# Kernel tuning notes

Measured on AMD Instinct MI355X. Metric: run time of the kernel, lower is better.

The kernel has to match this reference:

```python
import jax, jax.numpy as jnp
import numpy as np

N_NODES = 100000
N_EDGES = 1600000


def _deg_norm(idx, n):
    deg = jax.ops.segment_sum(jnp.ones(idx.shape[0], jnp.float32), idx, num_segments=n)
    return jnp.where(deg > 0, jax.lax.rsqrt(jnp.maximum(deg, 1.0)), 0.0)


def gcn_layer(src, dst, x, W, b):
    # DGL GraphConv, norm='both': D_in^{-1/2} A D_out^{-1/2} X W + b
    n = x.shape[0]
    h = x @ W                                   # project first (in >= out)
    norm_src = _deg_norm(src, n)                # out-degree norm at source
    norm_dst = _deg_norm(dst, n)                # in-degree norm at destination
    msg = (h * norm_src[:, None])[src]          # [E, d] gather
    agg = jax.ops.segment_sum(msg, dst, num_segments=n)
    return agg * norm_dst[:, None] + b


def setup_inputs() -> dict:
    key = jax.random.key(0)
    ks = jax.random.split(key, 6)
    in_f, h_f, n_cls = 256, 128, 64
    feat = jax.random.normal(ks[0], (N_NODES, in_f), jnp.float32)
    src = jax.random.randint(ks[1], (N_EDGES,), 0, N_NODES, jnp.int32)
    dst = jax.random.randint(ks[2], (N_EDGES,), 0, N_NODES, jnp.int32)
    W1 = jax.random.normal(ks[3], (in_f, h_f), jnp.float32) / np.sqrt(in_f)
    b1 = jnp.zeros((h_f,), jnp.float32)
    W2 = jax.random.normal(ks[4], (h_f, n_cls), jnp.float32) / np.sqrt(h_f)
    b2 = jnp.zeros((n_cls,), jnp.float32)
    return {"feat": feat, "src": src, "dst": dst, "W1": W1, "b1": b1, "W2": W2, "b2": b2}


def reference(feat, src, dst, W1, b1, W2, b2):
    h = gcn_layer(src, dst, feat, W1, b1)
    h = jax.nn.relu(h)
    h = gcn_layer(src, dst, h, W2, b2)
    return jax.nn.sigmoid(h)
```

## Files before the change

### kernel.cpp

```cpp
#include <hip/hip_runtime.h>
#include <cmath>

#define IN_F 256
#define H_F  128
#define N_CLS 64
#define SCAN_CHUNK 2048
#define EPB 4096
#define MAXBK 400

typedef __attribute__((ext_vector_type(8))) short bf16x8;
typedef __attribute__((ext_vector_type(4))) float f32x4;

__device__ __forceinline__ ushort f2bf(float x) {
  unsigned b = __builtin_bit_cast(unsigned, x);
  b += 0x7FFF + ((b >> 16) & 1);
  return (ushort)(b >> 16);
}

__global__ void conv_wT(const float* __restrict__ W, ushort* __restrict__ WT, int K, int N) {
  int i = blockIdx.x * blockDim.x + threadIdx.x;
  if (i >= K * N) return;
  int k = i / N, n = i % N;
  WT[n * K + k] = f2bf(W[i]);
}

__global__ __launch_bounds__(256) void hist_kernel(const int* __restrict__ src,
                                                   const int* __restrict__ dst,
                                                   int* __restrict__ hist,
                                                   int NBK, int NBLK, int E) {
  __shared__ int hD[MAXBK], hS[MAXBK];
  int t = threadIdx.x, blk = blockIdx.x;
  for (int b = t; b < NBK; b += 256) { hD[b] = 0; hS[b] = 0; }
  __syncthreads();
  int e0 = blk * EPB;
#pragma unroll
  for (int j = 0; j < EPB / 256; ++j) {
    int idx = e0 + j * 256 + t;
    if (idx < E) {
      atomicAdd(&hD[dst[idx] >> 8], 1);
      atomicAdd(&hS[src[idx] >> 8], 1);
    }
  }
  __syncthreads();
  for (int b = t; b < NBK; b += 256) {
    hist[(size_t)b * NBLK + blk] = hD[b];
    hist[(size_t)(NBK + b) * NBLK + blk] = hS[b];
  }
}

__device__ void excl_scan_lds(int* cnt, int* pos, int t, int nbk) {
  for (int b = t; b < nbk; b += 256) pos[b] = cnt[b];
  __syncthreads();
  for (int d = 1; d < 256; d <<= 1) {
    int u = (t < nbk && t >= d) ? pos[t - d] : 0;
    __syncthreads();
    if (t < nbk && t >= d) pos[t] += u;
    __syncthreads();
  }
  int m2 = nbk - 256;
  int s0 = (m2 > 0) ? pos[255] : 0;
  for (int d = 1; d < 256; d <<= 1) {
    int u = (m2 > 0 && t < m2 && t >= d) ? pos[256 + t - d] : 0;
    __syncthreads();
    if (m2 > 0 && t < m2 && t >= d) pos[256 + t] += u;
    __syncthreads();
  }
  if (m2 > 0 && t < m2) pos[256 + t] += s0;
  __syncthreads();
  for (int b = t; b < nbk; b += 256) pos[b] -= cnt[b];
  __syncthreads();
}

__global__ __launch_bounds__(256) void scatter_kernel(const int* __restrict__ src,
                                                      const int* __restrict__ dst,
                                                      const int* __restrict__ P,
                                                      int2* __restrict__ pairs_d,
                                                      int* __restrict__ srcs_s,
                                                      int NBK, int NBLK, int E) {
  __shared__ int cnt[MAXBK], pos[MAXBK], cur[MAXBK], gb[MAXBK];
  __shared__ int2 stage[EPB];
  int t = threadIdx.x, blk = blockIdx.x;
  int e0 = blk * EPB;
  int ne = E - e0; if (ne > EPB) ne = EPB;

  for (int b = t; b < NBK; b += 256) cnt[b] = 0;
  __syncthreads();
#pragma unroll
  for (int j = 0; j < EPB / 256; ++j) {
    int idx = e0 + j * 256 + t;
    if (idx < E) atomicAdd(&cnt[dst[idx] >> 8], 1);
  }
  __syncthreads();
  excl_scan_lds(cnt, pos, t, NBK);
  for (int b = t; b < NBK; b += 256) { cur[b] = pos[b]; gb[b] = P[(size_t)b * NBLK + blk]; }
  __syncthreads();
#pragma unroll
  for (int j = 0; j < EPB / 256; ++j) {
    int idx = e0 + j * 256 + t;
    if (idx < E) {
      int d = dst[idx];
      int r = atomicAdd(&cur[d >> 8], 1);
      stage[r] = make_int2(src[idx], d);
    }
  }
  __syncthreads();
  for (int i = t; i < ne; i += 256) {
    int2 p = stage[i];
    int b = p.y >> 8;
    pairs_d[gb[b] + (i - pos[b])] = p;
  }
  __syncthreads();

  int* stage_i = (int*)stage;
  for (int b = t; b < NBK; b += 256) cnt[b] = 0;
  __syncthreads();
#pragma unroll
  for (int j = 0; j < EPB / 256; ++j) {
    int idx = e0 + j * 256 + t;
    if (idx < E) atomicAdd(&cnt[src[idx] >> 8], 1);
  }
  __syncthreads();
  excl_scan_lds(cnt, pos, t, NBK);
  for (int b = t; b < NBK; b += 256) {
    cur[b] = pos[b];
    gb[b] = P[(size_t)(NBK + b) * NBLK + blk] - E;
  }
  __syncthreads();
#pragma unroll
  for (int j = 0; j < EPB / 256; ++j) {
    int idx = e0 + j * 256 + t;
    if (idx < E) {
      int s = src[idx];
      int r = atomicAdd(&cur[s >> 8], 1);
      stage_i[r] = s;
    }
  }
  __syncthreads();
  for (int i = t; i < ne; i += 256) {
    int s = stage_i[i];
    int b = s >> 8;
    srcs_s[gb[b] + (i - pos[b])] = s;
  }
}

__global__ __launch_bounds__(256) void csr_bucket(const int2* __restrict__ pairs_d,
                                                  const int* __restrict__ P,
                                                  int* __restrict__ row_off,
                                                  float* __restrict__ norm_d,
                                                  int* __restrict__ csr,
                                                  int NBK, int NBLK, int N, int E) {
  __shared__ int cnt[256], pos[256], cur[256];
  int b = blockIdx.x, t = threadIdx.x;
  int bstart = P[(size_t)b * NBLK];
  int bend = (b + 1 < NBK) ? P[(size_t)(b + 1) * NBLK] : E;
  cnt[t] = 0;
  __syncthreads();
  for (int i = bstart + t; i < bend; i += 256) atomicAdd(&cnt[pairs_d[i].y & 255], 1);
  __syncthreads();
  pos[t] = cnt[t];
  __syncthreads();
  for (int d = 1; d < 256; d <<= 1) {
    int u = (t >= d) ? pos[t - d] : 0;
    __syncthreads();
    if (t >= d) pos[t] += u;
    __syncthreads();
  }
  int excl = pos[t] - cnt[t];
  int node = b * 256 + t;
  if (node < N) {
    row_off[node] = bstart + excl;
    norm_d[node] = cnt[t] > 0 ? rsqrtf((float)cnt[t]) : 0.f;
  }
  if (b == NBK - 1 && t == 255) row_off[N] = E;
  cur[t] = excl;
  __syncthreads();
  for (int i = bstart + t; i < bend; i += 256) {
    int2 p = pairs_d[i];
    int r = atomicAdd(&cur[p.y & 255], 1);
    csr[bstart + r] = p.x;
  }
}

__global__ __launch_bounds__(256) void outdeg_bucket(const int* __restrict__ srcs_s,
                                                     const int* __restrict__ P,
                                                     float* __restrict__ norm_s,
                                                     int NBK, int NBLK, int N, int E) {
  __shared__ int cnt[256];
  int b = blockIdx.x, t = threadIdx.x;
  size_t SOFF = (size_t)NBK * NBLK;
  int sstart = P[SOFF + (size_t)b * NBLK] - E;
  int send = (b + 1 < NBK) ? P[SOFF + (size_t)(b + 1) * NBLK] - E : E;
  cnt[t] = 0;
  __syncthreads();
  for (int i = sstart + t; i < send; i += 256) atomicAdd(&cnt[srcs_s[i] & 255], 1);
  __syncthreads();
  int node = b * 256 + t;
  if (node < N) norm_s[node] = cnt[t] > 0 ? rsqrtf((float)cnt[t]) : 0.f;
}

__global__ void scan_part(const int* __restrict__ arr, int* __restrict__ bsum, int len) {
  int base = blockIdx.x * SCAN_CHUNK + threadIdx.x * 8;
  int s = 0;
#pragma unroll
  for (int j = 0; j < 8; ++j) {
    int i = base + j;
    if (i < len) s += arr[i];
  }
#pragma unroll
  for (int d = 1; d < 64; d <<= 1) s += __shfl_xor(s, d);
  __shared__ int ws[4];
  int lane = threadIdx.x & 63, w = threadIdx.x >> 6;
  if (lane == 0) ws[w] = s;
  __syncthreads();
  if (threadIdx.x == 0) bsum[blockIdx.x] = ws[0] + ws[1] + ws[2] + ws[3];
}

__global__ __launch_bounds__(1024) void scan_bsum(int* __restrict__ bsum, int nb) {
  __shared__ int sm[1024];
  int t = threadIdx.x;
  sm[t] = (t < nb) ? bsum[t] : 0;
  __syncthreads();
  for (int d = 1; d < 1024; d <<= 1) {
    int v = (t >= d) ? sm[t - d] : 0;
    __syncthreads();
    sm[t] += v;
    __syncthreads();
  }
  if (t < nb) bsum[t] = (t == 0) ? 0 : sm[t - 1];
}

__global__ void scan_final(const int* __restrict__ arr, const int* __restrict__ bsum_ex,
                           int* __restrict__ outp, int len, int total) {
  int base = blockIdx.x * SCAN_CHUNK + threadIdx.x * 8;
  int v[8], pre[8];
  int s = 0;
#pragma unroll
  for (int j = 0; j < 8; ++j) {
    int i = base + j;
    v[j] = (i < len) ? arr[i] : 0;
    pre[j] = s;
    s += v[j];
  }
  int lane = threadIdx.x & 63, w = threadIdx.x >> 6;
  int inc = s;
#pragma unroll
  for (int d = 1; d < 64; d <<= 1) {
    int u = __shfl_up(inc, d);
    if (lane >= d) inc += u;
  }
  __shared__ int wsum[4], woff[4];
  if (lane == 63) wsum[w] = inc;
  __syncthreads();
  if (threadIdx.x == 0) {
    int r = 0;
    for (int q = 0; q < 4; ++q) { woff[q] = r; r += wsum[q]; }
  }
  __syncthreads();
  int ex = (inc - s) + woff[w] + bsum_ex[blockIdx.x];
#pragma unroll
  for (int j = 0; j < 8; ++j) {
    int i = base + j;
    if (i < len) outp[i] = ex + pre[j];
  }
  if (blockIdx.x == 0 && threadIdx.x == 0) outp[len] = total;
}

__global__ __launch_bounds__(256) void mfma_gemm1(
    const float* __restrict__ A, const ushort* __restrict__ BT,
    const float* __restrict__ scale, ushort* __restrict__ C, int M) {
  constexpr int BM = 128, BN = 128, KTOT = 256, BK = 64, WM = 2, WN = 2;
  constexpr int FM = (BM / WM) / 16;
  constexpr int FN = (BN / WN) / 16;
  constexpr int ABYTES = BM * BK * 2;
  constexpr int BBYTES = BN * BK * 2;
  __shared__ char lds[ABYTES + BBYTES];
  char* Asm = lds;
  char* Bsm = lds + ABYTES;

  const int tid = threadIdx.x;
  const int lane = tid & 63;
  const int w = tid >> 6;
  const int wm = w / WN, wn = w % WN;
  const int m0 = blockIdx.x * BM;

  f32x4 acc[FM][FN];
#pragma unroll
  for (int m = 0; m < FM; ++m)
#pragma unroll
    for (int n = 0; n < FN; ++n) acc[m][n] = (f32x4){0.f, 0.f, 0.f, 0.f};

  const int ra = lane & 15;
  const int kg = lane >> 4;

  for (int kt = 0; kt < KTOT / BK; ++kt) {
#pragma unroll
    for (int s = 0; s < ABYTES / 4096; ++s) {
      int L = s * 4096 + tid * 16;
      int r = L >> 7;
      int slot = (L >> 4) & 7;
      int gr = m0 + r; if (gr >= M) gr = M - 1;
      const float4* gp = (const float4*)(A + (size_t)gr * KTOT + kt * BK + slot * 8);
      float4 va = gp[0], vb = gp[1];
      bf16x8 o;
      o[0] = (short)f2bf(va.x); o[1] = (short)f2bf(va.y);
      o[2] = (short)f2bf(va.z); o[3] = (short)f2bf(va.w);
      o[4] = (short)f2bf(vb.x); o[5] = (short)f2bf(vb.y);
      o[6] = (short)f2bf(vb.z); o[7] = (short)f2bf(vb.w);
      *(bf16x8*)(Asm + (L ^ ((r & 7) << 4))) = o;
    }
#pragma unroll
    for (int s = 0; s < BBYTES / 4096; ++s) {
      int L = s * 4096 + tid * 16;
      int r = L >> 7;
      int slot = (L >> 4) & 7;
      const char* gp = (const char*)BT + (size_t)r * (KTOT * 2) + kt * (BK * 2)
                     + ((slot * 16) ^ ((r & 7) << 4));
      __builtin_amdgcn_global_load_lds(
          (const __attribute__((address_space(1))) unsigned*)gp,
          (__attribute__((address_space(3))) unsigned*)(Bsm + L), 16, 0, 0);
    }
    __syncthreads();

#pragma unroll
    for (int ks = 0; ks < 2; ++ks) {
      bf16x8 af[FM], bfr[FN];
#pragma unroll
      for (int m = 0; m < FM; ++m) {
        int r = wm * (BM / WM) + m * 16 + ra;
        int cb = ks * 64 + kg * 16;
        af[m] = *(const bf16x8*)(Asm + r * 128 + (cb ^ ((r & 7) << 4)));
      }
#pragma unroll
      for (int n = 0; n < FN; ++n) {
        int c = wn * (BN / WN) + n * 16 + ra;
        int cb = ks * 64 + kg * 16;
        bfr[n] = *(const bf16x8*)(Bsm + c * 128 + (cb ^ ((c & 7) << 4)));
      }
#pragma unroll
      for (int m = 0; m < FM; ++m)
#pragma unroll
        for (int n = 0; n < FN; ++n)
          acc[m][n] = __builtin_amdgcn_mfma_f32_16x16x32_bf16(af[m], bfr[n], acc[m][n], 0, 0, 0);
    }
    __syncthreads();
  }

#pragma unroll
  for (int m = 0; m < FM; ++m) {
#pragma unroll
    for (int j = 0; j < 4; ++j) {
      int rl = wm * (BM / WM) + m * 16 + (lane >> 4) * 4 + j;
      int gr = m0 + rl;
      if (gr < M) {
        float sc = scale[gr];
#pragma unroll
        for (int n = 0; n < FN; ++n) {
          int c = wn * (BN / WN) + n * 16 + (lane & 15);
          C[(size_t)gr * BN + c] = f2bf(acc[m][n][j] * sc);
        }
      }
    }
  }
}

template<int BM, int BN, int KTOT, int WM, int WN>
__global__ __launch_bounds__(256) void mfma_gemm_scale(
    const ushort* __restrict__ A, const ushort* __restrict__ BT,
    const float* __restrict__ scale, ushort* __restrict__ C, int M) {
  constexpr int BK = 64;
  constexpr int FM = (BM / WM) / 16;
  constexpr int FN = (BN / WN) / 16;
  constexpr int ABYTES = BM * BK * 2;
  constexpr int BBYTES = BN * BK * 2;
  __shared__ char lds[ABYTES + BBYTES];
  char* Asm = lds;
  char* Bsm = lds + ABYTES;

  const int tid = threadIdx.x;
  const int lane = tid & 63;
  const int w = tid >> 6;
  const int wm = w / WN, wn = w % WN;
  const int m0 = blockIdx.x * BM;

  f32x4 acc[FM][FN];
#pragma unroll
  for (int m = 0; m < FM; ++m)
#pragma unroll
    for (int n = 0; n < FN; ++n) acc[m][n] = (f32x4){0.f, 0.f, 0.f, 0.f};

  const int ra = lane & 15;
  const int kg = lane >> 4;

  for (int kt = 0; kt < KTOT / BK; ++kt) {
#pragma unroll
    for (int s = 0; s < ABYTES / 4096; ++s) {
      int L = s * 4096 + tid * 16;
      int r = L >> 7;
      int slot = (L >> 4) & 7;
      int gr = m0 + r; if (gr >= M) gr = M - 1;
      const char* gp = (const char*)A + (size_t)gr * (KTOT * 2) + kt * (BK * 2)
                     + ((slot * 16) ^ ((r & 7) << 4));
      __builtin_amdgcn_global_load_lds(
          (const __attribute__((address_space(1))) unsigned*)gp,
          (__attribute__((address_space(3))) unsigned*)(Asm + L), 16, 0, 0);
    }
#pragma unroll
    for (int s = 0; s < BBYTES / 4096; ++s) {
      int L = s * 4096 + tid * 16;
      int r = L >> 7;
      int slot = (L >> 4) & 7;
      const char* gp = (const char*)BT + (size_t)r * (KTOT * 2) + kt * (BK * 2)
                     + ((slot * 16) ^ ((r & 7) << 4));
      __builtin_amdgcn_global_load_lds(
          (const __attribute__((address_space(1))) unsigned*)gp,
          (__attribute__((address_space(3))) unsigned*)(Bsm + L), 16, 0, 0);
    }
    __syncthreads();

#pragma unroll
    for (int ks = 0; ks < 2; ++ks) {
      bf16x8 af[FM], bfr[FN];
#pragma unroll
      for (int m = 0; m < FM; ++m) {
        int r = wm * (BM / WM) + m * 16 + ra;
        int cb = ks * 64 + kg * 16;
        af[m] = *(const bf16x8*)(Asm + r * 128 + (cb ^ ((r & 7) << 4)));
      }
#pragma unroll
      for (int n = 0; n < FN; ++n) {
        int c = wn * (BN / WN) + n * 16 + ra;
        int cb = ks * 64 + kg * 16;
        bfr[n] = *(const bf16x8*)(Bsm + c * 128 + (cb ^ ((c & 7) << 4)));
      }
#pragma unroll
      for (int m = 0; m < FM; ++m)
#pragma unroll
        for (int n = 0; n < FN; ++n)
          acc[m][n] = __builtin_amdgcn_mfma_f32_16x16x32_bf16(af[m], bfr[n], acc[m][n], 0, 0, 0);
    }
    __syncthreads();
  }

#pragma unroll
  for (int m = 0; m < FM; ++m) {
#pragma unroll
    for (int j = 0; j < 4; ++j) {
      int rl = wm * (BM / WM) + m * 16 + (lane >> 4) * 4 + j;
      int gr = m0 + rl;
      if (gr < M) {
        float sc = scale[gr];
#pragma unroll
        for (int n = 0; n < FN; ++n) {
          int c = wn * (BN / WN) + n * 16 + (lane & 15);
          C[(size_t)gr * BN + c] = f2bf(acc[m][n][j] * sc);
        }
      }
    }
  }
}

__global__ void gather1(const ushort* __restrict__ h1, const int* __restrict__ off,
                        const int* __restrict__ csr, const float* __restrict__ nd,
                        const float* __restrict__ b1, ushort* __restrict__ x2, int N) {
  int w = (blockIdx.x * blockDim.x + threadIdx.x) >> 6;
  int lane = threadIdx.x & 63;
  if (w >= N) return;
  int lo = off[w], hi = off[w + 1];
  const unsigned* h = (const unsigned*)h1;
  float sx = 0.f, sy = 0.f;
#define ACC1(u) { sx += __builtin_bit_cast(float, (u) << 16); \
                  sy += __builtin_bit_cast(float, (u) & 0xFFFF0000u); }
  int j = lo;
  for (; j + 16 <= hi; j += 16) {
    int s0 = csr[j+0], s1 = csr[j+1], s2 = csr[j+2], s3 = csr[j+3];
    int s4 = csr[j+4], s5 = csr[j+5], s6 = csr[j+6], s7 = csr[j+7];
    int s8 = csr[j+8], s9 = csr[j+9], sa = csr[j+10], sb = csr[j+11];
    int sc_ = csr[j+12], sd = csr[j+13], se = csr[j+14], sf = csr[j+15];
    unsigned u0 = h[(size_t)s0 * 64 + lane];
    unsigned u1 = h[(size_t)s1 * 64 + lane];
    unsigned u2 = h[(size_t)s2 * 64 + lane];
    unsigned u3 = h[(size_t)s3 * 64 + lane];
    unsigned u4 = h[(size_t)s4 * 64 + lane];
    unsigned u5 = h[(size_t)s5 * 64 + lane];
    unsigned u6 = h[(size_t)s6 * 64 + lane];
    unsigned u7 = h[(size_t)s7 * 64 + lane];
    unsigned u8 = h[(size_t)s8 * 64 + lane];
    unsigned u9 = h[(size_t)s9 * 64 + lane];
    unsigned ua = h[(size_t)sa * 64 + lane];
    unsigned ub = h[(size_t)sb * 64 + lane];
    unsigned uc = h[(size_t)sc_ * 64 + lane];
    unsigned ud = h[(size_t)sd * 64 + lane];
    unsigned ue = h[(size_t)se * 64 + lane];
    unsigned uf = h[(size_t)sf * 64 + lane];
    ACC1(u0) ACC1(u1) ACC1(u2) ACC1(u3) ACC1(u4) ACC1(u5) ACC1(u6) ACC1(u7)
    ACC1(u8) ACC1(u9) ACC1(ua) ACC1(ub) ACC1(uc) ACC1(ud) ACC1(ue) ACC1(uf)
  }
  for (; j + 4 <= hi; j += 4) {
    int s0 = csr[j+0], s1 = csr[j+1], s2 = csr[j+2], s3 = csr[j+3];
    unsigned u0 = h[(size_t)s0 * 64 + lane];
    unsigned u1 = h[(size_t)s1 * 64 + lane];
    unsigned u2 = h[(size_t)s2 * 64 + lane];
    unsigned u3 = h[(size_t)s3 * 64 + lane];
    ACC1(u0) ACC1(u1) ACC1(u2) ACC1(u3)
  }
  for (; j < hi; ++j) {
    int s = csr[j];
    unsigned u = h[(size_t)s * 64 + lane];
    ACC1(u)
  }
#undef ACC1
  float sc = nd[w];
  float2 bb = ((const float2*)b1)[lane];
  float ox = fmaxf(sx * sc + bb.x, 0.f);
  float oy = fmaxf(sy * sc + bb.y, 0.f);
  ushort2 o; o.x = f2bf(ox); o.y = f2bf(oy);
  ((ushort2*)x2)[(size_t)w * 64 + lane] = o;
}

__global__ void gather2(const ushort* __restrict__ h2, const int* __restrict__ off,
                        const int* __restrict__ csr, const float* __restrict__ nd,
                        const float* __restrict__ b2, float* __restrict__ out, int N) {
  int wv = (blockIdx.x * blockDim.x + threadIdx.x) >> 6;
  int lane = threadIdx.x & 63;
  int grp = lane >> 5;
  int sub = lane & 31;
  int node = wv * 2 + grp;
  if (node >= N) return;
  int lo = off[node], hi = off[node + 1];
  const unsigned* h = (const unsigned*)h2;
  float s0f = 0.f, s1f = 0.f;
#define ACC2(u) { s0f += __builtin_bit_cast(float, (u) << 16); \
                  s1f += __builtin_bit_cast(float, (u) & 0xFFFF0000u); }
  int j = lo;
  for (; j + 16 <= hi; j += 16) {
    int i0 = csr[j+0], i1 = csr[j+1], i2 = csr[j+2], i3 = csr[j+3];
    int i4 = csr[j+4], i5 = csr[j+5], i6 = csr[j+6], i7 = csr[j+7];
    int i8 = csr[j+8], i9 = csr[j+9], ia = csr[j+10], ib = csr[j+11];
    int ic = csr[j+12], id = csr[j+13], ie = csr[j+14], if_ = csr[j+15];
    unsigned u0 = h[(size_t)i0 * 32 + sub];
    unsigned u1 = h[(size_t)i1 * 32 + sub];
    unsigned u2 = h[(size_t)i2 * 32 + sub];
    unsigned u3 = h[(size_t)i3 * 32 + sub];
    unsigned u4 = h[(size_t)i4 * 32 + sub];
    unsigned u5 = h[(size_t)i5 * 32 + sub];
    unsigned u6 = h[(size_t)i6 * 32 + sub];
    unsigned u7 = h[(size_t)i7 * 32 + sub];
    unsigned u8 = h[(size_t)i8 * 32 + sub];
    unsigned u9 = h[(size_t)i9 * 32 + sub];
    unsigned ua = h[(size_t)ia * 32 + sub];
    unsigned ub = h[(size_t)ib * 32 + sub];
    unsigned uc = h[(size_t)ic * 32 + sub];
    unsigned ud = h[(size_t)id * 32 + sub];
    unsigned ue = h[(size_t)ie * 32 + sub];
    unsigned uf = h[(size_t)if_ * 32 + sub];
    ACC2(u0) ACC2(u1) ACC2(u2) ACC2(u3) ACC2(u4) ACC2(u5) ACC2(u6) ACC2(u7)
    ACC2(u8) ACC2(u9) ACC2(ua) ACC2(ub) ACC2(uc) ACC2(ud) ACC2(ue) ACC2(uf)
  }
  for (; j + 4 <= hi; j += 4) {
    int i0 = csr[j+0], i1 = csr[j+1], i2 = csr[j+2], i3 = csr[j+3];
    unsigned u0 = h[(size_t)i0 * 32 + sub];
    unsigned u1 = h[(size_t)i1 * 32 + sub];
    unsigned u2 = h[(size_t)i2 * 32 + sub];
    unsigned u3 = h[(size_t)i3 * 32 + sub];
    ACC2(u0) ACC2(u1) ACC2(u2) ACC2(u3)
  }
  for (; j < hi; ++j) {
    int i0 = csr[j];
    unsigned u = h[(size_t)i0 * 32 + sub];
    ACC2(u)
  }
#undef ACC2
  float scn = nd[node];
  float2 bb = ((const float2*)b2)[sub];
  float v0 = s0f * scn + bb.x;
  float v1 = s1f * scn + bb.y;
  float2 o;
  o.x = 1.f / (1.f + expf(-v0));
  o.y = 1.f / (1.f + expf(-v1));
  ((float2*)out)[(size_t)node * 32 + sub] = o;
}

extern "C" void kernel_launch(void* const* d_in, const int* in_sizes, int n_in,
                              void* d_out, int out_size, void* d_ws, size_t ws_size,
                              hipStream_t stream) {
  const float* feat = (const float*)d_in[0];
  const int*   src  = (const int*)d_in[1];
  const int*   dst  = (const int*)d_in[2];
  const float* W1   = (const float*)d_in[3];
  const float* b1   = (const float*)d_in[4];
  const float* W2   = (const float*)d_in[5];
  const float* b2   = (const float*)d_in[6];
  float* out = (float*)d_out;

  const int N = in_sizes[0] / IN_F;
  const int E = in_sizes[1];

  const int NBK  = (N + 255) >> 8;
  const int NBLK = (E + EPB - 1) / EPB;
  const int HLEN = 2 * NBK * NBLK;

  size_t off = 0;
  auto alloc = [&](size_t bytes) -> void* {
    void* p = (char*)d_ws + off;
    off = (off + bytes + 255) & ~(size_t)255;
    return p;
  };
  int*    hist    = (int*)alloc((size_t)HLEN * 4);
  int*    P       = (int*)alloc((size_t)(HLEN + 1) * 4);
  int*    bsum    = (int*)alloc((size_t)1024 * 4);
  int2*   pairs_d = (int2*)alloc((size_t)E * 8);
  int*    srcs_s  = (int*)alloc((size_t)E * 4);
  float*  norm_s  = (float*)alloc((size_t)N * 4);
  float*  norm_d  = (float*)alloc((size_t)N * 4);
  int*    row_off = (int*)alloc((size_t)(N + 1) * 4);
  int*    csr     = (int*)alloc((size_t)E * 4);
  ushort* w1t     = (ushort*)alloc((size_t)H_F * IN_F * 2);
  ushort* w2t     = (ushort*)alloc((size_t)N_CLS * H_F * 2);
  ushort* h1      = (ushort*)alloc((size_t)N * H_F * 2);
  ushort* x2bf    = (ushort*)alloc((size_t)N * H_F * 2);
  ushort* h2      = (ushort*)alloc((size_t)N * N_CLS * 2);
  (void)ws_size;

  conv_wT<<<(IN_F * H_F + 255) / 256, 256, 0, stream>>>(W1, w1t, IN_F, H_F);
  conv_wT<<<(H_F * N_CLS + 255) / 256, 256, 0, stream>>>(W2, w2t, H_F, N_CLS);

  hist_kernel<<<NBLK, 256, 0, stream>>>(src, dst, hist, NBK, NBLK, E);
  const int NBS = (HLEN + SCAN_CHUNK - 1) / SCAN_CHUNK;
  scan_part<<<NBS, 256, 0, stream>>>(hist, bsum, HLEN);
  scan_bsum<<<1, 1024, 0, stream>>>(bsum, NBS);
  scan_final<<<NBS, 256, 0, stream>>>(hist, bsum, P, HLEN, 2 * E);
  scatter_kernel<<<NBLK, 256, 0, stream>>>(src, dst, P, pairs_d, srcs_s, NBK, NBLK, E);
  csr_bucket<<<NBK, 256, 0, stream>>>(pairs_d, P, row_off, norm_d, csr, NBK, NBLK, N, E);
  outdeg_bucket<<<NBK, 256, 0, stream>>>(srcs_s, P, norm_s, NBK, NBLK, N, E);

  mfma_gemm1<<<(N + 127) / 128, 256, 0, stream>>>(feat, w1t, norm_s, h1, N);
  gather1<<<(N * 64 + 255) / 256, 256, 0, stream>>>(h1, row_off, csr, norm_d, b1, x2bf, N);

  mfma_gemm_scale<128, 64, 128, 2, 2><<<(N + 127) / 128, 256, 0, stream>>>(
      x2bf, w2t, norm_s, h2, N);
  int pairs = (N + 1) / 2;
  gather2<<<(pairs * 64 + 255) / 256, 256, 0, stream>>>(h2, row_off, csr, norm_d, b2, out, N);
}
```

Before: 229.1 us.

## Pack edge pairs, merge bucket kernels, and split layer-1 gather into feature halves

The sorted edge pairs are packed into one 32-bit word (source index shifted left by 8, low byte of destination), which halves scatter and CSR-build traffic. The in-degree and out-degree bucket kernels become one launch, as do the two weight conversions. The layer-1 gather now runs in two passes, each covering half the feature columns with two nodes per wavefront. This shrinks the per-pass working set of h1 to improve cache hit rate, at the cost of reading the CSR twice. The packing assumes source indices fit in 24 bits.

```diff
diff --git a/kernel.cpp b/kernel.cpp
--- a/kernel.cpp
+++ b/kernel.cpp
@@ -17,11 +17,17 @@
   return (ushort)(b >> 16);
 }
 
-__global__ void conv_wT(const float* __restrict__ W, ushort* __restrict__ WT, int K, int N) {
+__global__ void conv_w(const float* __restrict__ W1, ushort* __restrict__ W1T,
+                       const float* __restrict__ W2, ushort* __restrict__ W2T) {
   int i = blockIdx.x * blockDim.x + threadIdx.x;
-  if (i >= K * N) return;
-  int k = i / N, n = i % N;
-  WT[n * K + k] = f2bf(W[i]);
+  if (i < IN_F * H_F) {
+    int k = i / H_F, n = i % H_F;
+    W1T[n * IN_F + k] = f2bf(W1[i]);
+  } else if (i < IN_F * H_F + H_F * N_CLS) {
+    int j = i - IN_F * H_F;
+    int k = j / N_CLS, n = j % N_CLS;
+    W2T[n * H_F + k] = f2bf(W2[j]);
+  }
 }
 
 __global__ __launch_bounds__(256) void hist_kernel(const int* __restrict__ src,
@@ -74,11 +80,12 @@
 __global__ __launch_bounds__(256) void scatter_kernel(const int* __restrict__ src,
                                                       const int* __restrict__ dst,
                                                       const int* __restrict__ P,
-                                                      int2* __restrict__ pairs_d,
+                                                      int* __restrict__ pairs_pk,
                                                       int* __restrict__ srcs_s,
                                                       int NBK, int NBLK, int E) {
   __shared__ int cnt[MAXBK], pos[MAXBK], cur[MAXBK], gb[MAXBK];
-  __shared__ int2 stage[EPB];
+  __shared__ int stage_pk[EPB];
+  __shared__ ushort stage_b[EPB];
   int t = threadIdx.x, blk = blockIdx.x;
   int e0 = blk * EPB;
   int ne = E - e0; if (ne > EPB) ne = EPB;
@@ -100,18 +107,17 @@
     if (idx < E) {
       int d = dst[idx];
       int r = atomicAdd(&cur[d >> 8], 1);
-      stage[r] = make_int2(src[idx], d);
+      stage_pk[r] = (src[idx] << 8) | (d & 255);
+      stage_b[r] = (ushort)(d >> 8);
     }
   }
   __syncthreads();
   for (int i = t; i < ne; i += 256) {
-    int2 p = stage[i];
-    int b = p.y >> 8;
-    pairs_d[gb[b] + (i - pos[b])] = p;
-  }
-  __syncthreads();
-
-  int* stage_i = (int*)stage;
+    int b = stage_b[i];
+    pairs_pk[gb[b] + (i - pos[b])] = stage_pk[i];
+  }
+  __syncthreads();
+
   for (int b = t; b < NBK; b += 256) cnt[b] = 0;
   __syncthreads();
 #pragma unroll
@@ -132,30 +138,31 @@
     if (idx < E) {
       int s = src[idx];
       int r = atomicAdd(&cur[s >> 8], 1);
-      stage_i[r] = s;
+      stage_pk[r] = s;
     }
   }
   __syncthreads();
   for (int i = t; i < ne; i += 256) {
-    int s = stage_i[i];
+    int s = stage_pk[i];
     int b = s >> 8;
     srcs_s[gb[b] + (i - pos[b])] = s;
   }
 }
 
-__global__ __launch_bounds__(256) void csr_bucket(const int2* __restrict__ pairs_d,
-                                                  const int* __restrict__ P,
-                                                  int* __restrict__ row_off,
-                                                  float* __restrict__ norm_d,
-                                                  int* __restrict__ csr,
-                                                  int NBK, int NBLK, int N, int E) {
+__global__ __launch_bounds__(256) void csr_outdeg_bucket(
+    const int* __restrict__ pairs_pk, const int* __restrict__ srcs_s,
+    const int* __restrict__ P, int* __restrict__ row_off,
+    float* __restrict__ norm_d, float* __restrict__ norm_s,
+    int* __restrict__ csr, int NBK, int NBLK, int N, int E) {
   __shared__ int cnt[256], pos[256], cur[256];
   int b = blockIdx.x, t = threadIdx.x;
+  int node = b * 256 + t;
+
   int bstart = P[(size_t)b * NBLK];
   int bend = (b + 1 < NBK) ? P[(size_t)(b + 1) * NBLK] : E;
   cnt[t] = 0;
   __syncthreads();
-  for (int i = bstart + t; i < bend; i += 256) atomicAdd(&cnt[pairs_d[i].y & 255], 1);
+  for (int i = bstart + t; i < bend; i += 256) atomicAdd(&cnt[pairs_pk[i] & 255], 1);
   __syncthreads();
   pos[t] = cnt[t];
   __syncthreads();
@@ -166,7 +173,6 @@
     __syncthreads();
   }
   int excl = pos[t] - cnt[t];
-  int node = b * 256 + t;
   if (node < N) {
     row_off[node] = bstart + excl;
     norm_d[node] = cnt[t] > 0 ? rsqrtf((float)cnt[t]) : 0.f;
@@ -175,18 +181,12 @@
   cur[t] = excl;
   __syncthreads();
   for (int i = bstart + t; i < bend; i += 256) {
-    int2 p = pairs_d[i];
-    int r = atomicAdd(&cur[p.y & 255], 1);
-    csr[bstart + r] = p.x;
-  }
-}
-
-__global__ __launch_bounds__(256) void outdeg_bucket(const int* __restrict__ srcs_s,
-                                                     const int* __restrict__ P,
-                                                     float* __restrict__ norm_s,
-                                                     int NBK, int NBLK, int N, int E) {
-  __shared__ int cnt[256];
-  int b = blockIdx.x, t = threadIdx.x;
+    int pk = pairs_pk[i];
+    int r = atomicAdd(&cur[pk & 255], 1);
+    csr[bstart + r] = (int)((unsigned)pk >> 8);
+  }
+  __syncthreads();
+
   size_t SOFF = (size_t)NBK * NBLK;
   int sstart = P[SOFF + (size_t)b * NBLK] - E;
   int send = (b + 1 < NBK) ? P[SOFF + (size_t)(b + 1) * NBLK] - E : E;
@@ -194,7 +194,6 @@
   __syncthreads();
   for (int i = sstart + t; i < send; i += 256) atomicAdd(&cnt[srcs_s[i] & 255], 1);
   __syncthreads();
-  int node = b * 256 + t;
   if (node < N) norm_s[node] = cnt[t] > 0 ? rsqrtf((float)cnt[t]) : 0.f;
 }
 
@@ -459,62 +458,48 @@
   }
 }
 
-__global__ void gather1(const ushort* __restrict__ h1, const int* __restrict__ off,
-                        const int* __restrict__ csr, const float* __restrict__ nd,
-                        const float* __restrict__ b1, ushort* __restrict__ x2, int N) {
-  int w = (blockIdx.x * blockDim.x + threadIdx.x) >> 6;
+__global__ void gather1_ph(const ushort* __restrict__ h1, const int* __restrict__ off,
+                           const int* __restrict__ csr, const float* __restrict__ nd,
+                           const float* __restrict__ b1, ushort* __restrict__ x2,
+                           int N, int ph) {
+  int wv = (blockIdx.x * blockDim.x + threadIdx.x) >> 6;
   int lane = threadIdx.x & 63;
-  if (w >= N) return;
-  int lo = off[w], hi = off[w + 1];
+  int grp = lane >> 5;
+  int sub = lane & 31;
+  int node = wv * 2 + grp;
+  if (node >= N) return;
+  int lo = off[node], hi = off[node + 1];
   const unsigned* h = (const unsigned*)h1;
+  int base = ph * 32 + sub;
   float sx = 0.f, sy = 0.f;
 #define ACC1(u) { sx += __builtin_bit_cast(float, (u) << 16); \
                   sy += __builtin_bit_cast(float, (u) & 0xFFFF0000u); }
   int j = lo;
-  for (; j + 16 <= hi; j += 16) {
+  for (; j + 8 <= hi; j += 8) {
     int s0 = csr[j+0], s1 = csr[j+1], s2 = csr[j+2], s3 = csr[j+3];
     int s4 = csr[j+4], s5 = csr[j+5], s6 = csr[j+6], s7 = csr[j+7];
-    int s8 = csr[j+8], s9 = csr[j+9], sa = csr[j+10], sb = csr[j+11];
-    int sc_ = csr[j+12], sd = csr[j+13], se = csr[j+14], sf = csr[j+15];
-    unsigned u0 = h[(size_t)s0 * 64 + lane];
-    unsigned u1 = h[(size_t)s1 * 64 + lane];
-    unsigned u2 = h[(size_t)s2 * 64 + lane];
-    unsigned u3 = h[(size_t)s3 * 64 + lane];
-    unsigned u4 = h[(size_t)s4 * 64 + lane];
-    unsigned u5 = h[(size_t)s5 * 64 + lane];
-    unsigned u6 = h[(size_t)s6 * 64 + lane];
-    unsigned u7 = h[(size_t)s7 * 64 + lane];
-    unsigned u8 = h[(size_t)s8 * 64 + lane];
-    unsigned u9 = h[(size_t)s9 * 64 + lane];
-    unsigned ua = h[(size_t)sa * 64 + lane];
-    unsigned ub = h[(size_t)sb * 64 + lane];
-    unsigned uc = h[(size_t)sc_ * 64 + lane];
-    unsigned ud = h[(size_t)sd * 64 + lane];
-    unsigned ue = h[(size_t)se * 64 + lane];
-    unsigned uf = h[(size_t)sf * 64 + lane];
+    unsigned u0 = h[(size_t)s0 * 64 + base];
+    unsigned u1 = h[(size_t)s1 * 64 + base];
+    unsigned u2 = h[(size_t)s2 * 64 + base];
+    unsigned u3 = h[(size_t)s3 * 64 + base];
+    unsigned u4 = h[(size_t)s4 * 64 + base];
+    unsigned u5 = h[(size_t)s5 * 64 + base];
+    unsigned u6 = h[(size_t)s6 * 64 + base];
+    unsigned u7 = h[(size_t)s7 * 64 + base];
     ACC1(u0) ACC1(u1) ACC1(u2) ACC1(u3) ACC1(u4) ACC1(u5) ACC1(u6) ACC1(u7)
-    ACC1(u8) ACC1(u9) ACC1(ua) ACC1(ub) ACC1(uc) ACC1(ud) ACC1(ue) ACC1(uf)
-  }
-  for (; j + 4 <= hi; j += 4) {
-    int s0 = csr[j+0], s1 = csr[j+1], s2 = csr[j+2], s3 = csr[j+3];
-    unsigned u0 = h[(size_t)s0 * 64 + lane];
-    unsigned u1 = h[(size_t)s1 * 64 + lane];
-    unsigned u2 = h[(size_t)s2 * 64 + lane];
-    unsigned u3 = h[(size_t)s3 * 64 + lane];
-    ACC1(u0) ACC1(u1) ACC1(u2) ACC1(u3)
   }
   for (; j < hi; ++j) {
     int s = csr[j];
-    unsigned u = h[(size_t)s * 64 + lane];
+    unsigned u = h[(size_t)s * 64 + base];
     ACC1(u)
   }
 #undef ACC1
-  float sc = nd[w];
-  float2 bb = ((const float2*)b1)[lane];
+  float sc = nd[node];
+  float2 bb = ((const float2*)b1)[base];
   float ox = fmaxf(sx * sc + bb.x, 0.f);
   float oy = fmaxf(sy * sc + bb.y, 0.f);
   ushort2 o; o.x = f2bf(ox); o.y = f2bf(oy);
-  ((ushort2*)x2)[(size_t)w * 64 + lane] = o;
+  ((ushort2*)x2)[(size_t)node * 64 + base] = o;
 }
 
 __global__ void gather2(const ushort* __restrict__ h2, const int* __restrict__ off,
@@ -608,7 +593,7 @@
   int*    hist    = (int*)alloc((size_t)HLEN * 4);
   int*    P       = (int*)alloc((size_t)(HLEN + 1) * 4);
   int*    bsum    = (int*)alloc((size_t)1024 * 4);
-  int2*   pairs_d = (int2*)alloc((size_t)E * 8);
+  int*    pairs_pk= (int*)alloc((size_t)E * 4);
   int*    srcs_s  = (int*)alloc((size_t)E * 4);
   float*  norm_s  = (float*)alloc((size_t)N * 4);
   float*  norm_d  = (float*)alloc((size_t)N * 4);
@@ -621,23 +606,24 @@
   ushort* h2      = (ushort*)alloc((size_t)N * N_CLS * 2);
   (void)ws_size;
 
-  conv_wT<<<(IN_F * H_F + 255) / 256, 256, 0, stream>>>(W1, w1t, IN_F, H_F);
-  conv_wT<<<(H_F * N_CLS + 255) / 256, 256, 0, stream>>>(W2, w2t, H_F, N_CLS);
+  conv_w<<<(IN_F * H_F + H_F * N_CLS + 255) / 256, 256, 0, stream>>>(W1, w1t, W2, w2t);
 
   hist_kernel<<<NBLK, 256, 0, stream>>>(src, dst, hist, NBK, NBLK, E);
   const int NBS = (HLEN + SCAN_CHUNK - 1) / SCAN_CHUNK;
   scan_part<<<NBS, 256, 0, stream>>>(hist, bsum, HLEN);
   scan_bsum<<<1, 1024, 0, stream>>>(bsum, NBS);
   scan_final<<<NBS, 256, 0, stream>>>(hist, bsum, P, HLEN, 2 * E);
-  scatter_kernel<<<NBLK, 256, 0, stream>>>(src, dst, P, pairs_d, srcs_s, NBK, NBLK, E);
-  csr_bucket<<<NBK, 256, 0, stream>>>(pairs_d, P, row_off, norm_d, csr, NBK, NBLK, N, E);
-  outdeg_bucket<<<NBK, 256, 0, stream>>>(srcs_s, P, norm_s, NBK, NBLK, N, E);
+  scatter_kernel<<<NBLK, 256, 0, stream>>>(src, dst, P, pairs_pk, srcs_s, NBK, NBLK, E);
+  csr_outdeg_bucket<<<NBK, 256, 0, stream>>>(pairs_pk, srcs_s, P, row_off,
+                                             norm_d, norm_s, csr, NBK, NBLK, N, E);
 
   mfma_gemm1<<<(N + 127) / 128, 256, 0, stream>>>(feat, w1t, norm_s, h1, N);
-  gather1<<<(N * 64 + 255) / 256, 256, 0, stream>>>(h1, row_off, csr, norm_d, b1, x2bf, N);
+  int pairs = (N + 1) / 2;
+  int gblk = (pairs * 64 + 255) / 256;
+  gather1_ph<<<gblk, 256, 0, stream>>>(h1, row_off, csr, norm_d, b1, x2bf, N, 0);
+  gather1_ph<<<gblk, 256, 0, stream>>>(h1, row_off, csr, norm_d, b1, x2bf, N, 1);
 
   mfma_gemm_scale<128, 64, 128, 2, 2><<<(N + 127) / 128, 256, 0, stream>>>(
       x2bf, w2t, norm_s, h2, N);
-  int pairs = (N + 1) / 2;
   gather2<<<(pairs * 64 + 255) / 256, 256, 0, stream>>>(h2, row_off, csr, norm_d, b2, out, N);
 }
```

After: 246.2 us. 7.4% more time.
